# Kernel tuning notes

Measured on AMD Instinct MI355X. Metric: run time of the kernel, lower is better.

Reference implementation:

```python
import jax, jax.numpy as jnp
import numpy as np

BLOCK_M = 64
BLOCK_K = 64
THRES = 0.8


def setup_inputs() -> dict:
    key = jax.random.key(0)
    k1, k2 = jax.random.split(key)
    bsz, d_in, d_out = 8192, 4096, 4096
    x = jax.random.normal(k1, (bsz, d_in), dtype=jnp.float32)
    # kaiming_uniform_(a=sqrt(5)) on a (d_in, d_out) tensor -> bound = 1/sqrt(d_out)
    bound = 1.0 / np.sqrt(d_out)
    weight = jax.random.uniform(k2, (d_in, d_out), dtype=jnp.float32,
                                minval=-bound, maxval=bound)
    return {"x": x, "weight": weight}


def reference(x, weight):
    bsz, hidden = x.shape
    nm, nk = bsz // BLOCK_M, hidden // BLOCK_K
    # per-block average magnitude of activations: [nm, nk]
    blocks = jnp.abs(x).reshape(nm, BLOCK_M, nk, BLOCK_K)
    avg_mag = blocks.mean(axis=(1, 3))
    block_mask = avg_mag > THRES  # [nm, nk] bool
    # expand mask to element level and zero inactive activation blocks
    mask_elem = jnp.repeat(jnp.repeat(block_mask, BLOCK_M, axis=0), BLOCK_K, axis=1)
    x_masked = jnp.where(mask_elem, x, 0.0)
    # block-sparse masked GEMM (dense reference of the same math)
    return x_masked @ weight
```

## Files before the change

### kernel.cpp

```cpp
#include <hip/hip_runtime.h>
#include <hip/hip_bf16.h>
#include <stdint.h>

#define BSZ   8192
#define D_IN  4096
#define D_OUT 4096
#define NM    128
#define NK    64

typedef __bf16 bf16x8 __attribute__((ext_vector_type(8)));
typedef float  f32x4  __attribute__((ext_vector_type(4)));
typedef unsigned short ushort_t;

__device__ __forceinline__ ushort_t f2bf(float f) {
  union { __hip_bfloat16 h; ushort_t u; } c;
  c.h = __float2bfloat16(f);
  return c.u;
}

__device__ __forceinline__ bf16x8 ld_frag(const ushort_t* p) {
  union { uint4 u; bf16x8 b; } cv;
  cv.u = *(const uint4*)p;
  return cv.b;
}

__device__ __forceinline__ void glds16(const ushort_t* g, ushort_t* l) {
  __builtin_amdgcn_global_load_lds(
      (const __attribute__((address_space(1))) unsigned int*)g,
      (__attribute__((address_space(3))) unsigned int*)l,
      16, 0, 0);
}

__global__ __launch_bounds__(256) void mask_cast_kernel(
    const float* __restrict__ x, ushort_t* __restrict__ xb,
    int* __restrict__ mask) {
  const int kblk = blockIdx.x;
  const int mblk = blockIdx.y;
  const int tid  = threadIdx.x;
  const int lane = tid & 63;
  const int wv   = tid >> 6;
  const size_t row0 = (size_t)mblk * 64;
  const int    col0 = kblk * 64;

  float4 v[4];
  double s = 0.0;
#pragma unroll
  for (int i = 0; i < 4; ++i) {
    int j = i * 256 + tid;
    int r = j >> 4;
    int c = (j & 15) * 4;
    v[i] = *(const float4*)(x + (row0 + r) * D_IN + col0 + c);
    s += (double)fabsf(v[i].x) + (double)fabsf(v[i].y) +
         (double)fabsf(v[i].z) + (double)fabsf(v[i].w);
  }

#pragma unroll
  for (int off = 32; off > 0; off >>= 1) {
    union { double d; int i2[2]; } u;
    u.d = s;
    u.i2[0] = __shfl_xor(u.i2[0], off, 64);
    u.i2[1] = __shfl_xor(u.i2[1], off, 64);
    s += u.d;
  }

  __shared__ double wsum[4];
  __shared__ int mflag;
  if (lane == 0) wsum[wv] = s;
  __syncthreads();
  if (tid == 0) {
    double tot = wsum[0] + wsum[1] + wsum[2] + wsum[3];
    float avg = (float)(tot * (1.0 / 4096.0));
    int m = (avg > 0.8f) ? 1 : 0;
    mflag = m;
    mask[mblk * NK + kblk] = m;
  }
  __syncthreads();

  if (mflag) {
#pragma unroll
    for (int i = 0; i < 4; ++i) {
      int j = i * 256 + tid;
      int r = j >> 4;
      int c = (j & 15) * 4;
      ushort4 o = make_ushort4(f2bf(v[i].x), f2bf(v[i].y),
                               f2bf(v[i].z), f2bf(v[i].w));
      *(ushort4*)(xb + (row0 + r) * D_IN + col0 + c) = o;
    }
  }
}

__global__ __launch_bounds__(256) void wcast_transpose_kernel(
    const float* __restrict__ w, ushort_t* __restrict__ wT) {
  const int ntile = blockIdx.x;
  const int ktile = blockIdx.y;
  const int tid   = threadIdx.x;
  const int k0 = ktile * 64, n0 = ntile * 64;

  __shared__ ushort_t t[64][65];

#pragma unroll
  for (int i = 0; i < 4; ++i) {
    int j = i * 256 + tid;
    int r = j >> 4;
    int c = (j & 15) * 4;
    float4 v = *(const float4*)(w + (size_t)(k0 + r) * D_OUT + n0 + c);
    t[r][c + 0] = f2bf(v.x);
    t[r][c + 1] = f2bf(v.y);
    t[r][c + 2] = f2bf(v.z);
    t[r][c + 3] = f2bf(v.w);
  }
  __syncthreads();
#pragma unroll
  for (int i = 0; i < 4; ++i) {
    int j = i * 256 + tid;
    int r = j >> 4;
    int c = (j & 15) * 4;
    ushort4 o = make_ushort4(t[c + 0][r], t[c + 1][r], t[c + 2][r], t[c + 3][r]);
    *(ushort4*)(wT + (size_t)(n0 + r) * D_IN + k0 + c) = o;
  }
}

__global__ __launch_bounds__(512) void bsp_gemm_kernel(
    const ushort_t* __restrict__ xb, const ushort_t* __restrict__ wT,
    const int* __restrict__ mask, float* __restrict__ out) {
  const int ntile = blockIdx.x;
  const int mpair = blockIdx.y;
  const int tid   = threadIdx.x;
  const int lane  = tid & 63;
  const int wv    = tid >> 6;
  const int mi    = wv >> 2;
  const int nj    = wv & 3;
  const int m0 = mpair * 128;
  const int n0 = ntile * 256;

  __shared__ ushort_t As[128 * 64];
  __shared__ ushort_t Bs[256 * 64];
  __shared__ int nact;
  __shared__ unsigned char klist[64];

  if (tid < 64) {
    const int* mrow = mask + (size_t)(mpair * 2) * NK;
    int a0 = (mrow[tid] != 0) ? 1 : 0;
    int a1 = (mrow[NK + tid] != 0) ? 1 : 0;
    unsigned long long u = __ballot(a0 | a1);
    if (a0 | a1) {
      int pos = __popcll(u & ((1ull << tid) - 1ull));
      klist[pos] = (unsigned char)(tid | (a0 << 6) | (a1 << 7));
    }
    if (tid == 0) nact = (int)__popcll(u);
  }
  __syncthreads();
  const int na = nact;

  f32x4 acc[4][4] = {};

  const int lr  = lane >> 3;
  const int lcs = ((lane & 7) ^ (lane >> 3)) * 8;
  const int q   = lane >> 4;
  const int l15 = lane & 15;
  const int sx  = l15 & 7;

  for (int ki = 0; ki < na; ++ki) {
    const int e   = klist[ki];
    const int kb  = e & 63;
    const int k0  = kb * 64;
    const int act = (e >> (6 + mi)) & 1;

    if (act) {
#pragma unroll
      for (int t = 0; t < 2; ++t) {
        int rb = wv * 16 + t * 8;
        glds16(xb + (size_t)(m0 + rb + lr) * D_IN + k0 + lcs, &As[rb * 64]);
      }
    }
#pragma unroll
    for (int t = 0; t < 4; ++t) {
      int rb = wv * 32 + t * 8;
      glds16(wT + (size_t)(n0 + rb + lr) * D_IN + k0 + lcs, &Bs[rb * 64]);
    }
    __syncthreads();

    if (act) {
#pragma unroll
      for (int c = 0; c < 2; ++c) {
        const int sw = ((c * 4 + q) ^ sx) * 8;
        bf16x8 a[4], b[4];
#pragma unroll
        for (int i = 0; i < 4; ++i)
          a[i] = ld_frag(&As[(mi * 64 + i * 16 + l15) * 64 + sw]);
#pragma unroll
        for (int j = 0; j < 4; ++j)
          b[j] = ld_frag(&Bs[(nj * 64 + j * 16 + l15) * 64 + sw]);
#pragma unroll
        for (int i = 0; i < 4; ++i)
#pragma unroll
          for (int j = 0; j < 4; ++j)
            acc[i][j] = __builtin_amdgcn_mfma_f32_16x16x32_bf16(
                a[i], b[j], acc[i][j], 0, 0, 0);
      }
    }
    __syncthreads();
  }

#pragma unroll
  for (int i = 0; i < 4; ++i) {
#pragma unroll
    for (int j = 0; j < 4; ++j) {
#pragma unroll
      for (int r = 0; r < 4; ++r) {
        int row = m0 + mi * 64 + i * 16 + q * 4 + r;
        int col = n0 + nj * 64 + j * 16 + l15;
        out[(size_t)row * D_OUT + col] = acc[i][j][r];
      }
    }
  }
}

extern "C" void kernel_launch(void* const* d_in, const int* in_sizes, int n_in,
                              void* d_out, int out_size, void* d_ws, size_t ws_size,
                              hipStream_t stream) {
  const float* x = (const float*)d_in[0];
  const float* w = (const float*)d_in[1];

  ushort_t* xb  = (ushort_t*)d_ws;
  ushort_t* wT  = (ushort_t*)((char*)d_ws + (size_t)BSZ * D_IN * 2);
  int*      msk = (int*)((char*)d_ws + (size_t)BSZ * D_IN * 2 + (size_t)D_IN * D_OUT * 2);
  float*    out = (float*)d_out;

  hipLaunchKernelGGL(mask_cast_kernel, dim3(NK, NM), dim3(256), 0, stream,
                     x, xb, msk);
  hipLaunchKernelGGL(wcast_transpose_kernel, dim3(64, 64), dim3(256), 0, stream,
                     w, wT);
  hipLaunchKernelGGL(bsp_gemm_kernel, dim3(D_OUT / 256, NM / 2), dim3(512), 0, stream,
                     xb, wT, msk, out);
}
```

Before: 421.3 us.

## Double-buffer LDS tiles in block-sparse GEMM to overlap loads with MFMA

Doubles the A and B LDS buffers and issues the global-to-LDS loads for the next active k-block before computing the current one. Explicit s_waitcnt vmcnt counts matched to the number of outstanding loads replace the full barrier wait, so memory latency can be hidden behind MFMA work. The cost is doubled LDS use (96KB), which may reduce occupancy. The waitcnt counting is also fragile: the count varies per wave depending on whether its A tile is active, and it assumes the compiler emits no other vector memory ops in between.

```diff
diff --git a/kernel.cpp b/kernel.cpp
--- a/kernel.cpp
+++ b/kernel.cpp
@@ -133,8 +133,8 @@
   const int m0 = mpair * 128;
   const int n0 = ntile * 256;
 
-  __shared__ ushort_t As[128 * 64];
-  __shared__ ushort_t Bs[256 * 64];
+  __shared__ ushort_t As[2][128 * 64];
+  __shared__ ushort_t Bs[2][256 * 64];
   __shared__ int nact;
   __shared__ unsigned char klist[64];
 
@@ -160,37 +160,51 @@
   const int l15 = lane & 15;
   const int sx  = l15 & 7;
 
-  for (int ki = 0; ki < na; ++ki) {
-    const int e   = klist[ki];
-    const int kb  = e & 63;
-    const int k0  = kb * 64;
-    const int act = (e >> (6 + mi)) & 1;
-
-    if (act) {
+  auto stage = [&](int ki, int buf) -> int {
+    const int e  = klist[ki];
+    const int k0 = (e & 63) * 64;
+#pragma unroll
+    for (int t = 0; t < 4; ++t) {
+      int rb = wv * 32 + t * 8;
+      glds16(wT + (size_t)(n0 + rb + lr) * D_IN + k0 + lcs, &Bs[buf][rb * 64]);
+    }
+    if ((e >> (6 + mi)) & 1) {
 #pragma unroll
       for (int t = 0; t < 2; ++t) {
         int rb = wv * 16 + t * 8;
-        glds16(xb + (size_t)(m0 + rb + lr) * D_IN + k0 + lcs, &As[rb * 64]);
+        glds16(xb + (size_t)(m0 + rb + lr) * D_IN + k0 + lcs, &As[buf][rb * 64]);
       }
-    }
-#pragma unroll
-    for (int t = 0; t < 4; ++t) {
-      int rb = wv * 32 + t * 8;
-      glds16(wT + (size_t)(n0 + rb + lr) * D_IN + k0 + lcs, &Bs[rb * 64]);
-    }
-    __syncthreads();
-
-    if (act) {
+      return 6;
+    }
+    return 4;
+  };
+
+  int cur = 0;
+  if (na > 0) stage(0, 0);
+
+  for (int ki = 0; ki < na; ++ki) {
+    int c_next = 0;
+    if (ki + 1 < na) c_next = stage(ki + 1, cur ^ 1);
+
+    if (c_next == 6)      asm volatile("s_waitcnt vmcnt(6)" ::: "memory");
+    else if (c_next == 4) asm volatile("s_waitcnt vmcnt(4)" ::: "memory");
+    else                  asm volatile("s_waitcnt vmcnt(0)" ::: "memory");
+
+    __builtin_amdgcn_s_barrier();
+    asm volatile("" ::: "memory");
+
+    const int e = klist[ki];
+    if ((e >> (6 + mi)) & 1) {
 #pragma unroll
       for (int c = 0; c < 2; ++c) {
         const int sw = ((c * 4 + q) ^ sx) * 8;
         bf16x8 a[4], b[4];
 #pragma unroll
         for (int i = 0; i < 4; ++i)
-          a[i] = ld_frag(&As[(mi * 64 + i * 16 + l15) * 64 + sw]);
+          a[i] = ld_frag(&As[cur][(mi * 64 + i * 16 + l15) * 64 + sw]);
 #pragma unroll
         for (int j = 0; j < 4; ++j)
-          b[j] = ld_frag(&Bs[(nj * 64 + j * 16 + l15) * 64 + sw]);
+          b[j] = ld_frag(&Bs[cur][(nj * 64 + j * 16 + l15) * 64 + sw]);
 #pragma unroll
         for (int i = 0; i < 4; ++i)
 #pragma unroll
@@ -199,7 +213,10 @@
                 a[i], b[j], acc[i][j], 0, 0, 0);
       }
     }
-    __syncthreads();
+
+    asm volatile("" ::: "memory");
+    __builtin_amdgcn_s_barrier();
+    cur ^= 1;
   }
 
 #pragma unroll
```

Measured after the change: 452.0 us. 7.3% more time.
